# Kernel tuning notes

Measured on AMD Instinct MI355X. Metric: run time of the kernel, lower is better.

Reference implementation:

```python
import jax, jax.numpy as jnp
import numpy as np

N, R, B, OUT, STD = 512, 4, 65536, 512, 0.01


def setup_inputs() -> dict:
    key = jax.random.key(0)
    ks = jax.random.split(key, 6)
    return {
        "x": jax.random.normal(ks[0], (B, N), jnp.float32),
        "G": jax.random.normal(ks[1], (N, R), jnp.float32) * STD,
        "H": jax.random.normal(ks[2], (N, R), jnp.float32) * STD,
        "b1": jax.random.normal(ks[3], (N,), jnp.float32) * STD,
        "W2": jax.random.normal(ks[4], (N, OUT), jnp.float32) * STD,
        "b2": jax.random.normal(ks[5], (OUT,), jnp.float32) * STD,
    }


def _shift_A(v):
    # Z_1 v: circular shift down with corner +1 (Toeplitz-like operator A)
    return jnp.concatenate([v[-1:], v[:-1]], axis=0)


def _shift_BT(v):
    # Z_{-1}^T v: shift up with corner -1 (Toeplitz-like operator B^T)
    return jnp.concatenate([v[1:], -v[:1]], axis=0)


def _krylov(shift_fn, V):
    # K[j, :, i] = A^j v_i, shape (n, n, r)
    def step(v, _):
        return shift_fn(v), v
    _, K = jax.lax.scan(step, V, None, length=V.shape[0])
    return K


def krylov_recon(G, H):
    # W = sum_i Krylov(Z_1, g_i) @ Krylov(Z_{-1}^T, h_i)^T, shape (n, n)
    KA = _krylov(_shift_A, G)   # (n, n, r)
    KB = _krylov(_shift_BT, H)  # (n, n, r)
    return jnp.einsum('jai,jbi->ab', KA, KB)


def reference(x, G, H, b1, W2, b2):
    W = krylov_recon(G, H)                 # (n, n) structured matrix
    h = jax.nn.relu(x @ W + b1)            # (B, n)
    return h @ W2 + b2                     # (B, out)
```

## Files before the change

kernel.cpp:

```cpp
#include <hip/hip_runtime.h>
#include <hip/hip_bf16.h>
#include <stdint.h>


typedef __attribute__((ext_vector_type(8))) short bf16x8;
typedef __attribute__((ext_vector_type(4))) float f32x4;
typedef __attribute__((ext_vector_type(4))) unsigned int u32x4;

__device__ __forceinline__ unsigned short f2bf(float f) {
  return __builtin_bit_cast(unsigned short, __float2bfloat16(f));
}

__global__ void build_w_partials(const float* __restrict__ G, const float* __restrict__ H,
                                 float* __restrict__ Wp) {
  __shared__ float4 Gs[512];
  __shared__ float4 Hs[512];
  const int t = threadIdx.x;
  const float4* G4 = (const float4*)G;
  const float4* H4 = (const float4*)H;
  for (int i = t; i < 512; i += 256) { Gs[i] = G4[i]; Hs[i] = H4[i]; }
  __syncthreads();

  const int blk  = blockIdx.x;
  const int tile = blk >> 2;
  const int jc   = blk & 3;
  const int a0 = (tile >> 3) << 6;
  const int b0 = (tile & 7) << 6;
  const int ab = a0 + ((t >> 4) << 2);
  const int bb = b0 + ((t & 15) << 2);

  float acc[4][4] = {};
  const int j0 = jc << 7;
  for (int jj = 0; jj < 128; ++jj) {
    const int j = j0 + jj;
    float4 Ga[4], Hb[4];
#pragma unroll
    for (int r = 0; r < 4; ++r) Ga[r] = Gs[(ab + r - j) & 511];
#pragma unroll
    for (int c = 0; c < 4; ++c) {
      const int idx = bb + c + j;
      const float s = (idx >= 512) ? -1.f : 1.f;
      const float4 hv = Hs[idx & 511];
      Hb[c].x = hv.x * s; Hb[c].y = hv.y * s; Hb[c].z = hv.z * s; Hb[c].w = hv.w * s;
    }
#pragma unroll
    for (int r = 0; r < 4; ++r)
#pragma unroll
      for (int c = 0; c < 4; ++c)
        acc[r][c] += Ga[r].x * Hb[c].x + Ga[r].y * Hb[c].y +
                     Ga[r].z * Hb[c].z + Ga[r].w * Hb[c].w;
  }

  float* outp = Wp + (size_t)jc * 262144;
#pragma unroll
  for (int r = 0; r < 4; ++r)
#pragma unroll
    for (int c = 0; c < 4; ++c)
      outp[(size_t)(ab + r) * 512 + (bb + c)] = acc[r][c];
}

__global__ void reduce_transpose_w(const float* __restrict__ Wp, unsigned short* __restrict__ Wt) {
  const int idx = blockIdx.x * 256 + threadIdx.x;
  const int b = idx >> 9, a = idx & 511;
  const size_t o = (size_t)a * 512 + b;
  float s = Wp[o] + Wp[o + 262144] + Wp[o + 524288] + Wp[o + 786432];
  Wt[(size_t)b * 512 + a] = f2bf(s);
}

__global__ void transpose_convert_w2(const float* __restrict__ W2, unsigned short* __restrict__ W2t) {
  const int idx = blockIdx.x * 256 + threadIdx.x;
  const int n = idx >> 9, k = idx & 511;
  W2t[(size_t)n * 512 + k] = f2bf(W2[(size_t)k * 512 + n]);
}

template <bool AF32>
__global__ __launch_bounds__(512, 2) void gemm_pipe(
    const void* __restrict__ Ap, const unsigned short* __restrict__ Bt,
    const float* __restrict__ bias, void* __restrict__ Cp) {
  constexpr int NT    = 16;
  constexpr int AHALF = AF32 ? 16384 : 8192;
  constexpr int BHALF = 8192;
  constexpr int SLOT  = 2 * AHALF + 2 * BHALF;
  constexpr int NAG   = AF32 ? 2 : 1;

  __shared__ __attribute__((aligned(16))) char lds[3 * SLOT];

  const int tid  = threadIdx.x;
  const int lane = tid & 63;
  const int w    = tid >> 6;
  const int wm   = w & 1;
  const int wn   = w >> 1;
  const int lr   = lane & 15;
  const int lq   = lane >> 4;

  const int bid = (int)blockIdx.x;
  const int wg  = (bid & 7) * 64 + (bid >> 3);
  const int m0  = (wg >> 1) << 8;
  const int n0  = (wg & 1) << 8;

  float bv[4];
#pragma unroll
  for (int ni = 0; ni < 4; ++ni) bv[ni] = bias[n0 + wn * 64 + ni * 16 + lr];
  asm volatile("s_waitcnt vmcnt(0)" ::: "memory");

  size_t aOff[NAG];
  if constexpr (AF32) {
#pragma unroll
    for (int i = 0; i < 2; ++i) {
      const int c = i * 512 + tid, row = c >> 3, cr = c & 7;
      aOff[i] = (size_t)row * 2048 + (size_t)((cr ^ (row & 7)) << 4);
    }
  } else {
    const int rp = tid >> 3, sub = tid & 7;
    const int r = 2 * rp + (sub >> 2), cg = (sub & 3) ^ (rp & 3);
    aOff[0] = (size_t)r * 1024 + (size_t)(cg << 4);
  }
  size_t bOff;
  {
    const int rp = tid >> 3, sub = tid & 7;
    const int r = 2 * rp + (sub >> 2), cg = (sub & 3) ^ (rp & 3);
    bOff = (size_t)r * 1024 + (size_t)(cg << 4);
  }
  const char* aBase = (const char*)Ap + (size_t)m0 * (AF32 ? 2048 : 1024);
  const char* bBase = (const char*)Bt + (size_t)n0 * 1024;

  auto stageA = [&](int kt, int sl, int h) {
#pragma unroll
    for (int i = 0; i < NAG; ++i)
      __builtin_amdgcn_global_load_lds(
        (const __attribute__((address_space(1))) void*)
          (aBase + (size_t)h * 128 * (AF32 ? 2048 : 1024) + (size_t)kt * (AF32 ? 128 : 64) + aOff[i]),
        (__attribute__((address_space(3))) void*)(lds + sl * SLOT + h * AHALF + i * 8192 + w * 1024),
        16, 0, 0);
  };
  auto stageB = [&](int kt, int sl, int h) {
    __builtin_amdgcn_global_load_lds(
      (const __attribute__((address_space(1))) void*)
        (bBase + (size_t)h * 131072 + (size_t)kt * 64 + bOff),
      (__attribute__((address_space(3))) void*)(lds + sl * SLOT + 2 * AHALF + h * BHALF + w * 1024),
      16, 0, 0);
  };

  int offA8[8], offB4[4];
#pragma unroll
  for (int mi = 0; mi < 8; ++mi) {
    const int r = mi * 16 + lr;
    if constexpr (AF32)
      offA8[mi] = r * 128 + (((2 * lq) ^ (r & 7)) << 4);
    else
      offA8[mi] = (r >> 1) * 128 + (r & 1) * 64 + ((lq ^ ((r >> 1) & 3)) << 4);
  }
#pragma unroll
  for (int ni = 0; ni < 4; ++ni) {
    const int rb = (wn & 1) * 64 + ni * 16 + lr;
    offB4[ni] = (rb >> 1) * 128 + (rb & 1) * 64 + ((lq ^ ((rb >> 1) & 3)) << 4);
  }

  f32x4 acc[8][4];
  const f32x4 vz = {0.f, 0.f, 0.f, 0.f};
#pragma unroll
  for (int i = 0; i < 8; ++i)
#pragma unroll
    for (int j = 0; j < 4; ++j) acc[i][j] = vz;

  stageA(0, 0, 0); stageA(0, 0, 1); stageB(0, 0, 0); stageB(0, 0, 1);
  stageA(1, 1, 0); stageA(1, 1, 1); stageB(1, 1, 0); stageB(1, 1, 1);
  if constexpr (AF32) asm volatile("s_waitcnt vmcnt(6)" ::: "memory");
  else                asm volatile("s_waitcnt vmcnt(4)" ::: "memory");
  __builtin_amdgcn_s_barrier();
  __builtin_amdgcn_sched_barrier(0);

  for (int t = 0; t < NT; ++t) {
    const int s  = t % 3;
    const int s2 = (t + 2) % 3;
    const char* aB = lds + s * SLOT + wm * AHALF;
    const char* bB = lds + s * SLOT + 2 * AHALF + (wn >> 1) * BHALF;
    bf16x8 bfr[4];

    {
#pragma unroll
      for (int ni = 0; ni < 4; ++ni) bfr[ni] = *(const bf16x8*)(bB + offB4[ni]);
      bf16x8 afr[4];
      f32x4 lo[4], hi[4];
      if constexpr (AF32) {
#pragma unroll
        for (int k = 0; k < 4; ++k) {
          lo[k] = *(const f32x4*)(aB + offA8[k]);
          hi[k] = *(const f32x4*)(aB + (offA8[k] ^ 16));
        }
      } else {
#pragma unroll
        for (int k = 0; k < 4; ++k) afr[k] = *(const bf16x8*)(aB + offA8[k]);
      }
      if (t + 2 < NT) { stageA(t + 2, s2, 0); stageB(t + 2, s2, 0); }
      __builtin_amdgcn_s_barrier();
      asm volatile("s_waitcnt lgkmcnt(0)" ::: "memory");
      __builtin_amdgcn_sched_barrier(0);
      if constexpr (AF32) {
#pragma unroll
        for (int k = 0; k < 4; ++k) {
          unsigned int w0, w1, w2, w3;
          asm("v_cvt_pk_bf16_f32 %0, %1, %2" : "=v"(w0) : "v"(lo[k].x), "v"(lo[k].y));
          asm("v_cvt_pk_bf16_f32 %0, %1, %2" : "=v"(w1) : "v"(lo[k].z), "v"(lo[k].w));
          asm("v_cvt_pk_bf16_f32 %0, %1, %2" : "=v"(w2) : "v"(hi[k].x), "v"(hi[k].y));
          asm("v_cvt_pk_bf16_f32 %0, %1, %2" : "=v"(w3) : "v"(hi[k].z), "v"(hi[k].w));
          u32x4 pw = {w0, w1, w2, w3};
          afr[k] = __builtin_bit_cast(bf16x8, pw);
        }
      }
      __builtin_amdgcn_s_setprio(1);
#pragma unroll
      for (int k = 0; k < 4; ++k)
#pragma unroll
        for (int ni = 0; ni < 4; ++ni)
          acc[k][ni] = __builtin_amdgcn_mfma_f32_16x16x32_bf16(afr[k], bfr[ni], acc[k][ni], 0, 0, 0);
      __builtin_amdgcn_s_setprio(0);
      __builtin_amdgcn_s_barrier();
      __builtin_amdgcn_sched_barrier(0);
    }

    {
      bf16x8 afr[4];
      f32x4 lo[4], hi[4];
      if constexpr (AF32) {
#pragma unroll
        for (int k = 0; k < 4; ++k) {
          lo[k] = *(const f32x4*)(aB + offA8[4 + k]);
          hi[k] = *(const f32x4*)(aB + (offA8[4 + k] ^ 16));
        }
      } else {
#pragma unroll
        for (int k = 0; k < 4; ++k) afr[k] = *(const bf16x8*)(aB + offA8[4 + k]);
      }
      if (t + 2 < NT) { stageA(t + 2, s2, 1); stageB(t + 2, s2, 1); }
      __builtin_amdgcn_s_barrier();
      asm volatile("s_waitcnt lgkmcnt(0)" ::: "memory");
      __builtin_amdgcn_sched_barrier(0);
      if constexpr (AF32) {
#pragma unroll
        for (int k = 0; k < 4; ++k) {
          unsigned int w0, w1, w2, w3;
          asm("v_cvt_pk_bf16_f32 %0, %1, %2" : "=v"(w0) : "v"(lo[k].x), "v"(lo[k].y));
          asm("v_cvt_pk_bf16_f32 %0, %1, %2" : "=v"(w1) : "v"(lo[k].z), "v"(lo[k].w));
          asm("v_cvt_pk_bf16_f32 %0, %1, %2" : "=v"(w2) : "v"(hi[k].x), "v"(hi[k].y));
          asm("v_cvt_pk_bf16_f32 %0, %1, %2" : "=v"(w3) : "v"(hi[k].z), "v"(hi[k].w));
          u32x4 pw = {w0, w1, w2, w3};
          afr[k] = __builtin_bit_cast(bf16x8, pw);
        }
      }
      __builtin_amdgcn_s_setprio(1);
#pragma unroll
      for (int k = 0; k < 4; ++k)
#pragma unroll
        for (int ni = 0; ni < 4; ++ni)
          acc[4 + k][ni] = __builtin_amdgcn_mfma_f32_16x16x32_bf16(afr[k], bfr[ni], acc[4 + k][ni], 0, 0, 0);
      __builtin_amdgcn_s_setprio(0);
      if (t < NT - 2) {
        if constexpr (AF32) asm volatile("s_waitcnt vmcnt(6)" ::: "memory");
        else                asm volatile("s_waitcnt vmcnt(4)" ::: "memory");
      } else if (t == NT - 2) {
        asm volatile("s_waitcnt vmcnt(0)" ::: "memory");
      }
      __builtin_amdgcn_s_barrier();
      __builtin_amdgcn_sched_barrier(0);
    }
  }

#pragma unroll
  for (int ni = 0; ni < 4; ++ni) {
    const int gc = n0 + wn * 64 + ni * 16 + lr;
#pragma unroll
    for (int mi = 0; mi < 8; ++mi) {
      const int gr = m0 + wm * 128 + mi * 16 + lq * 4;
      const f32x4 v = acc[mi][ni];
#pragma unroll
      for (int i = 0; i < 4; ++i) {
        const float val = v[i] + bv[ni];
        if constexpr (AF32)
          ((unsigned short*)Cp)[(size_t)(gr + i) * 512 + gc] = f2bf(val > 0.f ? val : 0.f);
        else
          ((float*)Cp)[(size_t)(gr + i) * 512 + gc] = val;
      }
    }
  }
}

extern "C" void kernel_launch(void* const* d_in, const int* in_sizes, int n_in,
                              void* d_out, int out_size, void* d_ws, size_t ws_size,
                              hipStream_t stream) {
  (void)in_sizes; (void)n_in; (void)out_size; (void)ws_size;
  const float* x  = (const float*)d_in[0];
  const float* G  = (const float*)d_in[1];
  const float* H  = (const float*)d_in[2];
  const float* b1 = (const float*)d_in[3];
  const float* W2 = (const float*)d_in[4];
  const float* b2 = (const float*)d_in[5];
  float* out = (float*)d_out;

  char* ws = (char*)d_ws;
  unsigned short* h   = (unsigned short*)ws;
  unsigned short* Wt  = (unsigned short*)(ws + 67108864);
  unsigned short* W2t = (unsigned short*)(ws + 67633152);
  float*          Wp  = (float*)(ws + 68157440);

  build_w_partials<<<256, 256, 0, stream>>>(G, H, Wp);
  reduce_transpose_w<<<1024, 256, 0, stream>>>(Wp, Wt);
  transpose_convert_w2<<<1024, 256, 0, stream>>>(W2, W2t);
  gemm_pipe<true><<<512, 512, 0, stream>>>((const void*)x, Wt, b1, (void*)h);
  gemm_pipe<false><<<512, 512, 0, stream>>>((const void*)h, W2t, b2, (void*)out);
}
```

Before: 174.6 us.

## Restructure GEMM LDS staging into separate A/B rings with deeper prefetch

Splits the shared-memory staging into separate A and B ring buffers. The bf16-A GEMM now uses four slots with prefetch distance three, while the fp32-A GEMM keeps three slots and distance two. Each tile is loaded whole instead of as two halves, with A issued in the first half-step and B in the second, and the k-loop is fully unrolled. The aim is to hide global-load latency better, at the cost of more LDS, which may reduce occupancy under the two-blocks-per-CU launch bound.

Measured after the change: 168.7 us. 3.4% less time.

```diff
diff --git a/kernel.cpp b/kernel.cpp
--- a/kernel.cpp
+++ b/kernel.cpp
@@ -78,12 +78,15 @@
     const void* __restrict__ Ap, const unsigned short* __restrict__ Bt,
     const float* __restrict__ bias, void* __restrict__ Cp) {
   constexpr int NT    = 16;
-  constexpr int AHALF = AF32 ? 16384 : 8192;
-  constexpr int BHALF = 8192;
-  constexpr int SLOT  = 2 * AHALF + 2 * BHALF;
-  constexpr int NAG   = AF32 ? 2 : 1;
-
-  __shared__ __attribute__((aligned(16))) char lds[3 * SLOT];
+  constexpr int ASLOT = AF32 ? 32768 : 16384;
+  constexpr int ARING = AF32 ? 3 : 4;
+  constexpr int BSLOT = 16384;
+  constexpr int BRING = AF32 ? 3 : 4;
+  constexpr int DIST  = AF32 ? 2 : 3;
+  constexpr int NAG   = AF32 ? 4 : 2;
+  constexpr int BBASE = ARING * ASLOT;
+
+  __shared__ __attribute__((aligned(16))) char lds[ARING * ASLOT + BRING * BSLOT];
 
   const int tid  = threadIdx.x;
   const int lane = tid & 63;
@@ -103,57 +106,69 @@
   for (int ni = 0; ni < 4; ++ni) bv[ni] = bias[n0 + wn * 64 + ni * 16 + lr];
   asm volatile("s_waitcnt vmcnt(0)" ::: "memory");
 
-  size_t aOff[NAG];
+  size_t aSrcOff[NAG];
   if constexpr (AF32) {
 #pragma unroll
+    for (int i = 0; i < 4; ++i) {
+      const int r = i * 64 + (tid >> 3);
+      const int s = tid & 7;
+      const int c = s ^ (r & 7);
+      aSrcOff[i] = (size_t)r * 2048 + (size_t)(c << 4);
+    }
+  } else {
+#pragma unroll
     for (int i = 0; i < 2; ++i) {
-      const int c = i * 512 + tid, row = c >> 3, cr = c & 7;
-      aOff[i] = (size_t)row * 2048 + (size_t)((cr ^ (row & 7)) << 4);
-    }
-  } else {
-    const int rp = tid >> 3, sub = tid & 7;
-    const int r = 2 * rp + (sub >> 2), cg = (sub & 3) ^ (rp & 3);
-    aOff[0] = (size_t)r * 1024 + (size_t)(cg << 4);
-  }
-  size_t bOff;
-  {
-    const int rp = tid >> 3, sub = tid & 7;
-    const int r = 2 * rp + (sub >> 2), cg = (sub & 3) ^ (rp & 3);
-    bOff = (size_t)r * 1024 + (size_t)(cg << 4);
+      const int r = i * 128 + (tid >> 2);
+      const int s = tid & 3;
+      const int c = s ^ ((r >> 1) & 3);
+      aSrcOff[i] = (size_t)r * 1024 + (size_t)(c << 4);
+    }
+  }
+  size_t bSrcOff[2];
+#pragma unroll
+  for (int i = 0; i < 2; ++i) {
+    const int r = i * 128 + (tid >> 2);
+    const int s = tid & 3;
+    const int c = s ^ ((r >> 1) & 3);
+    bSrcOff[i] = (size_t)r * 1024 + (size_t)(c << 4);
   }
   const char* aBase = (const char*)Ap + (size_t)m0 * (AF32 ? 2048 : 1024);
   const char* bBase = (const char*)Bt + (size_t)n0 * 1024;
 
-  auto stageA = [&](int kt, int sl, int h) {
+  auto stageA = [&](int kt) {
+    const int sl = kt % ARING;
 #pragma unroll
     for (int i = 0; i < NAG; ++i)
       __builtin_amdgcn_global_load_lds(
         (const __attribute__((address_space(1))) void*)
-          (aBase + (size_t)h * 128 * (AF32 ? 2048 : 1024) + (size_t)kt * (AF32 ? 128 : 64) + aOff[i]),
-        (__attribute__((address_space(3))) void*)(lds + sl * SLOT + h * AHALF + i * 8192 + w * 1024),
+          (aBase + aSrcOff[i] + (size_t)kt * (AF32 ? 128 : 64)),
+        (__attribute__((address_space(3))) void*)(lds + sl * ASLOT + i * 8192 + w * 1024),
         16, 0, 0);
   };
-  auto stageB = [&](int kt, int sl, int h) {
-    __builtin_amdgcn_global_load_lds(
-      (const __attribute__((address_space(1))) void*)
-        (bBase + (size_t)h * 131072 + (size_t)kt * 64 + bOff),
-      (__attribute__((address_space(3))) void*)(lds + sl * SLOT + 2 * AHALF + h * BHALF + w * 1024),
-      16, 0, 0);
+  auto stageB = [&](int kt) {
+    const int sl = kt % BRING;
+#pragma unroll
+    for (int i = 0; i < 2; ++i)
+      __builtin_amdgcn_global_load_lds(
+        (const __attribute__((address_space(1))) void*)
+          (bBase + bSrcOff[i] + (size_t)kt * 64),
+        (__attribute__((address_space(3))) void*)(lds + BBASE + sl * BSLOT + i * 8192 + w * 1024),
+        16, 0, 0);
   };
 
-  int offA8[8], offB4[4];
+  int offA[8], offB[4];
 #pragma unroll
   for (int mi = 0; mi < 8; ++mi) {
-    const int r = mi * 16 + lr;
+    const int r = wm * 128 + mi * 16 + lr;
     if constexpr (AF32)
-      offA8[mi] = r * 128 + (((2 * lq) ^ (r & 7)) << 4);
+      offA[mi] = r * 128 + (((2 * lq) ^ (r & 7)) << 4);
     else
-      offA8[mi] = (r >> 1) * 128 + (r & 1) * 64 + ((lq ^ ((r >> 1) & 3)) << 4);
+      offA[mi] = r * 64 + ((lq ^ ((r >> 1) & 3)) << 4);
   }
 #pragma unroll
   for (int ni = 0; ni < 4; ++ni) {
-    const int rb = (wn & 1) * 64 + ni * 16 + lr;
-    offB4[ni] = (rb >> 1) * 128 + (rb & 1) * 64 + ((lq ^ ((rb >> 1) & 3)) << 4);
+    const int rb = wn * 64 + ni * 16 + lr;
+    offB[ni] = rb * 64 + ((lq ^ ((rb >> 1) & 3)) << 4);
   }
 
   f32x4 acc[8][4];
@@ -163,36 +178,35 @@
 #pragma unroll
     for (int j = 0; j < 4; ++j) acc[i][j] = vz;
 
-  stageA(0, 0, 0); stageA(0, 0, 1); stageB(0, 0, 0); stageB(0, 0, 1);
-  stageA(1, 1, 0); stageA(1, 1, 1); stageB(1, 1, 0); stageB(1, 1, 1);
+  stageA(0); stageB(0); stageA(1); stageB(1);
+  if constexpr (!AF32) { stageA(2); stageB(2); }
   if constexpr (AF32) asm volatile("s_waitcnt vmcnt(6)" ::: "memory");
-  else                asm volatile("s_waitcnt vmcnt(4)" ::: "memory");
+  else                asm volatile("s_waitcnt vmcnt(8)" ::: "memory");
   __builtin_amdgcn_s_barrier();
   __builtin_amdgcn_sched_barrier(0);
 
+#pragma unroll
   for (int t = 0; t < NT; ++t) {
-    const int s  = t % 3;
-    const int s2 = (t + 2) % 3;
-    const char* aB = lds + s * SLOT + wm * AHALF;
-    const char* bB = lds + s * SLOT + 2 * AHALF + (wn >> 1) * BHALF;
+    const char* aS = lds + (t % ARING) * ASLOT;
+    const char* bS = lds + BBASE + (t % BRING) * BSLOT;
     bf16x8 bfr[4];
 
     {
 #pragma unroll
-      for (int ni = 0; ni < 4; ++ni) bfr[ni] = *(const bf16x8*)(bB + offB4[ni]);
+      for (int ni = 0; ni < 4; ++ni) bfr[ni] = *(const bf16x8*)(bS + offB[ni]);
       bf16x8 afr[4];
       f32x4 lo[4], hi[4];
       if constexpr (AF32) {
 #pragma unroll
         for (int k = 0; k < 4; ++k) {
-          lo[k] = *(const f32x4*)(aB + offA8[k]);
-          hi[k] = *(const f32x4*)(aB + (offA8[k] ^ 16));
+          lo[k] = *(const f32x4*)(aS + offA[k]);
+          hi[k] = *(const f32x4*)(aS + (offA[k] ^ 16));
         }
       } else {
 #pragma unroll
-        for (int k = 0; k < 4; ++k) afr[k] = *(const bf16x8*)(aB + offA8[k]);
-      }
-      if (t + 2 < NT) { stageA(t + 2, s2, 0); stageB(t + 2, s2, 0); }
+        for (int k = 0; k < 4; ++k) afr[k] = *(const bf16x8*)(aS + offA[k]);
+      }
+      if (t + DIST < NT) stageA(t + DIST);
       __builtin_amdgcn_s_barrier();
       asm volatile("s_waitcnt lgkmcnt(0)" ::: "memory");
       __builtin_amdgcn_sched_barrier(0);
@@ -225,14 +239,14 @@
       if constexpr (AF32) {
 #pragma unroll
         for (int k = 0; k < 4; ++k) {
-          lo[k] = *(const f32x4*)(aB + offA8[4 + k]);
-          hi[k] = *(const f32x4*)(aB + (offA8[4 + k] ^ 16));
+          lo[k] = *(const f32x4*)(aS + offA[4 + k]);
+          hi[k] = *(const f32x4*)(aS + (offA[4 + k] ^ 16));
         }
       } else {
 #pragma unroll
-        for (int k = 0; k < 4; ++k) afr[k] = *(const bf16x8*)(aB + offA8[4 + k]);
-      }
-      if (t + 2 < NT) { stageA(t + 2, s2, 1); stageB(t + 2, s2, 1); }
+        for (int k = 0; k < 4; ++k) afr[k] = *(const bf16x8*)(aS + offA[4 + k]);
+      }
+      if (t + DIST < NT) stageB(t + DIST);
       __builtin_amdgcn_s_barrier();
       asm volatile("s_waitcnt lgkmcnt(0)" ::: "memory");
       __builtin_amdgcn_sched_barrier(0);
@@ -255,11 +269,13 @@
         for (int ni = 0; ni < 4; ++ni)
           acc[4 + k][ni] = __builtin_amdgcn_mfma_f32_16x16x32_bf16(afr[k], bfr[ni], acc[4 + k][ni], 0, 0, 0);
       __builtin_amdgcn_s_setprio(0);
-      if (t < NT - 2) {
-        if constexpr (AF32) asm volatile("s_waitcnt vmcnt(6)" ::: "memory");
-        else                asm volatile("s_waitcnt vmcnt(4)" ::: "memory");
-      } else if (t == NT - 2) {
-        asm volatile("s_waitcnt vmcnt(0)" ::: "memory");
+      if constexpr (AF32) {
+        if (t <= NT - 3)      asm volatile("s_waitcnt vmcnt(6)" ::: "memory");
+        else if (t == NT - 2) asm volatile("s_waitcnt vmcnt(0)" ::: "memory");
+      } else {
+        if (t <= NT - 4)      asm volatile("s_waitcnt vmcnt(8)" ::: "memory");
+        else if (t == NT - 3) asm volatile("s_waitcnt vmcnt(4)" ::: "memory");
+        else if (t == NT - 2) asm volatile("s_waitcnt vmcnt(0)" ::: "memory");
       }
       __builtin_amdgcn_s_barrier();
       __builtin_amdgcn_sched_barrier(0);
```
